# Kernel tuning notes

Hardware: AMD Instinct MI355X
Metric: run time of the kernel (lower is better)

## Reference

```python
import jax, jax.numpy as jnp
import numpy as np

V_F_LEN = 512
I_F_LEN = 256
F_LEN = V_F_LEN + I_F_LEN  # 768, GRU input_size == hidden_size == f_len
NUM_LAYERS = 2
B, S = 64, 256


def _uniform(key, shape, scale):
    return jax.random.uniform(key, shape, jnp.float32, -scale, scale)


def setup_inputs() -> dict:
    key = jax.random.key(0)
    ks = jax.random.split(key, 16)
    fv = jax.random.normal(ks[0], (B, S, V_F_LEN), jnp.float32)
    fi = jax.random.normal(ks[1], (B, S, I_F_LEN), jnp.float32)
    ts = jax.random.uniform(ks[2], (B, S), jnp.float32)
    H = F_LEN
    sc = 1.0 / np.sqrt(H)
    # GRU params, PyTorch layout: [num_layers, 3H, H] with gate order (r, z, n)
    W_ih = _uniform(ks[3], (NUM_LAYERS, 3 * H, H), sc)
    W_hh = _uniform(ks[4], (NUM_LAYERS, 3 * H, H), sc)
    b_ih = _uniform(ks[5], (NUM_LAYERS, 3 * H), sc)
    b_hh = _uniform(ks[6], (NUM_LAYERS, 3 * H), sc)
    sc1 = 1.0 / np.sqrt(H)
    sc2 = 1.0 / np.sqrt(128)
    W1 = _uniform(ks[7], (128, H), sc1)
    b1 = _uniform(ks[8], (128,), sc1)
    W2 = _uniform(ks[9], (6, 128), sc2)
    b2 = _uniform(ks[10], (6,), sc2)
    return {"fv": fv, "fi": fi, "ts": ts, "W_ih": W_ih, "W_hh": W_hh,
            "b_ih": b_ih, "b_hh": b_hh, "W1": W1, "b1": b1, "W2": W2, "b2": b2}


def _gru_layer(x, h0, Wih, Whh, bih, bhh):
    # x: [B, S, H], h0: [B, H]
    def step(h, x_t):
        gi = x_t @ Wih.T + bih          # [B, 3H]
        gh = h @ Whh.T + bhh
        ir, iz, in_ = jnp.split(gi, 3, axis=-1)
        hr, hz, hn = jnp.split(gh, 3, axis=-1)
        r = jax.nn.sigmoid(ir + hr)
        z = jax.nn.sigmoid(iz + hz)
        n = jnp.tanh(in_ + r * hn)
        h_new = (1.0 - z) * n + z * h
        return h_new, h_new
    h_last, ys = jax.lax.scan(step, h0, jnp.swapaxes(x, 0, 1))  # ys: [S, B, H]
    return jnp.swapaxes(ys, 0, 1), h_last


def reference(fv, fi, ts, W_ih, W_hh, b_ih, b_hh, W1, b1, W2, b2):
    # FusionModule with fuse_method='cat': concatenate along feature dim
    fused = jnp.concatenate([fv, fi], axis=-1)  # [B, S, F_LEN]
    bsz = fused.shape[0]
    h0 = jnp.zeros((NUM_LAYERS, bsz, F_LEN), fused.dtype)
    # Note: the torch module feeds one timestep at a time, but the math is
    # identical to running the full sequence through the multilayer GRU.
    x = fused
    h_finals = []
    for l in range(NUM_LAYERS):
        x, h_l = _gru_layer(x, h0[l], W_ih[l], W_hh[l], b_ih[l], b_hh[l])
        h_finals.append(h_l)
    h_n = jnp.stack(h_finals, axis=0)  # [L, B, H]
    hdn = x @ W1.T + b1
    hdn = jnp.where(hdn >= 0, hdn, 0.1 * hdn)  # LeakyReLU(0.1)
    pose = hdn @ W2.T + b2                      # [B, S, 6]
    return (pose, h_n)
```

## Files before the change

kernel.cpp:

```cpp
#include <hip/hip_runtime.h>
#include <stdint.h>


typedef __attribute__((ext_vector_type(8))) short bf16x8;
typedef __attribute__((ext_vector_type(4))) short bf16x4;
typedef __attribute__((ext_vector_type(4))) float f32x4;

#define H_   768
#define TH3  2304
#define BATCH 64
#define SEQ  256
#define SLAB (BATCH * H_)
#define WROW 772
#define FL_STRIDE 128

__device__ __forceinline__ uint16_t f2b(float f) {
  union { float f; uint32_t u; } v; v.f = f;
  uint32_t u = v.u;
  return (uint16_t)((u + 0x7FFFu + ((u >> 16) & 1u)) >> 16);
}

__device__ __forceinline__ f32x4 mfma16(bf16x8 a, bf16x8 b, f32x4 c) {
  return __builtin_amdgcn_mfma_f32_16x16x32_bf16(a, b, c, 0, 0, 0);
}

__device__ __forceinline__ bf16x8 ldB(const uint16_t* p) {
  bf16x4 lo = *reinterpret_cast<const bf16x4*>(p);
  bf16x4 hi = *reinterpret_cast<const bf16x4*>(p + 4);
  bf16x8 r;
  r[0] = lo[0]; r[1] = lo[1]; r[2] = lo[2]; r[3] = lo[3];
  r[4] = hi[0]; r[5] = hi[1]; r[6] = hi[2]; r[7] = hi[3];
  return r;
}

__device__ __forceinline__ void pollFlags48(const int* base, int lane) {
  const int* fp = base + (lane < 48 ? lane : 0);
  int spins = 0;
  for (;;) {
    int v = __hip_atomic_load(fp, __ATOMIC_RELAXED, __HIP_MEMORY_SCOPE_AGENT);
    if (lane >= 48) v = 1;
    if (__all(v != 0)) break;
    if (++spins > (1 << 16)) break;
    __builtin_amdgcn_s_sleep(1);
  }
  __builtin_amdgcn_sched_barrier(0);
}

__device__ __forceinline__ float fsig(float x) {
  return 1.0f / (1.0f + __expf(-x));
}
__device__ __forceinline__ float ftanh(float x) {
  x = fminf(fmaxf(x, -15.0f), 15.0f);
  float e = __expf(2.0f * x);
  return (e - 1.0f) / (e + 1.0f);
}

__global__ __launch_bounds__(256) void prep_kernel(
    const float* __restrict__ fv, const float* __restrict__ fi,
    const float* __restrict__ W1,
    uint16_t* __restrict__ Xbf, int* __restrict__ flags, uint16_t* __restrict__ W1b)
{
  const int NX = SEQ * SLAB;
  const int NC = 257 * FL_STRIDE;
  const int NW = 128 * H_;
  const int total = NX + NC + NW;
  for (int idx = blockIdx.x * blockDim.x + threadIdx.x; idx < total;
       idx += gridDim.x * blockDim.x) {
    if (idx < NX) {
      int s = idx / SLAB;
      int rem = idx - s * SLAB;
      int b = rem / H_;
      int h = rem - b * H_;
      float val = (h < 512) ? fv[((size_t)b * SEQ + s) * 512 + h]
                            : fi[((size_t)b * SEQ + s) * 256 + (h - 512)];
      Xbf[idx] = f2b(val);
    } else if (idx < NX + NC) {
      flags[idx - NX] = 0;
    } else {
      int k = idx - NX - NC;
      W1b[k] = f2b(W1[k]);
    }
  }
}

__global__ __launch_bounds__(512) void gru_persist(
    const float* __restrict__ Wih, const float* __restrict__ Whh,
    const float* __restrict__ bih, const float* __restrict__ bhh,
    const uint16_t* __restrict__ Xbf, uint16_t* __restrict__ Y0, uint16_t* __restrict__ Y1,
    int* __restrict__ flags, float* __restrict__ out_hn)
{
  __shared__ __attribute__((aligned(16))) uint16_t Wx[48 * WROW];
  __shared__ __attribute__((aligned(16))) uint16_t Wh[48 * WROW];
  __shared__ float ghbuf[64 * 48];
  __shared__ float bI[48];
  __shared__ float bH[48];

  const int bid   = blockIdx.x;
  const int slice = bid % 48;
  const int layer = bid / 48;
  const int tid  = threadIdx.x;
  const int lane = tid & 63;
  const int wid  = tid >> 6;
  const int isGh = wid >> 2;
  const int mblk = wid & 3;
  const int n16  = lane & 15;
  const int kg   = lane >> 4;

  const float* wx_g = Wih + (size_t)layer * TH3 * H_;
  const float* wh_g = Whh + (size_t)layer * TH3 * H_;
  for (int idx = tid; idx < 48 * H_; idx += 512) {
    int lr = idx / H_;
    int c  = idx - lr * H_;
    int gate = lr >> 4, j = lr & 15;
    size_t grow = (size_t)(gate * H_ + slice * 16 + j);
    Wx[lr * WROW + c] = f2b(wx_g[grow * H_ + c]);
    Wh[lr * WROW + c] = f2b(wh_g[grow * H_ + c]);
  }
  if (tid < 48) {
    int gate = tid >> 4, j = tid & 15;
    bI[tid] = bih[layer * TH3 + gate * H_ + slice * 16 + j];
    bH[tid] = bhh[layer * TH3 + gate * H_ + slice * 16 + j];
  }
  __syncthreads();

  uint16_t* Yown = layer ? Y1 : Y0;
  const uint16_t* Wh_base = Wh + (size_t)n16 * WROW + kg * 8;
  const uint16_t* Wx_base = Wx + (size_t)n16 * WROW + kg * 8;

  f32x4 xac0 = {0,0,0,0}, xac1 = {0,0,0,0}, xac2 = {0,0,0,0};
  float hp[4] = {0.0f, 0.0f, 0.0f, 0.0f};

  for (int i = 0; i <= 256; ++i) {
    const bool active = (layer == 0) ? (i < 256) : (i >= 1);
    const bool firstA = (layer == 0) ? (i == 0) : (i == 1);

    if (active) {
      if (isGh) {
        if (firstA) {
          #pragma unroll
          for (int q = 0; q < 4; ++q) {
            int bi = mblk * 16 + 4 * kg + q;
            ghbuf[bi * 48 +      n16] = 0.0f;
            ghbuf[bi * 48 + 16 + n16] = 0.0f;
            ghbuf[bi * 48 + 32 + n16] = 0.0f;
          }
        } else {
          pollFlags48(flags + (size_t)(i - 1) * FL_STRIDE + layer * 64, lane);
          const uint16_t* hs = (layer == 0) ? (Y0 + (size_t)i * SLAB)
                                            : (Y1 + (size_t)(i - 1) * SLAB);
          const uint16_t* ap = hs + (size_t)(mblk * 16 + n16) * H_ + kg * 8;
          f32x4 a0 = {0,0,0,0}, a1 = {0,0,0,0}, a2 = {0,0,0,0};
          #pragma unroll
          for (int ks = 0; ks < 24; ++ks) {
            bf16x8 av  = *reinterpret_cast<const bf16x8*>(ap + ks * 32);
            bf16x8 bv0 = ldB(Wh_base + ks * 32);
            bf16x8 bv1 = ldB(Wh_base + 16 * WROW + ks * 32);
            bf16x8 bv2 = ldB(Wh_base + 32 * WROW + ks * 32);
            a0 = mfma16(av, bv0, a0);
            a1 = mfma16(av, bv1, a1);
            a2 = mfma16(av, bv2, a2);
          }
          #pragma unroll
          for (int q = 0; q < 4; ++q) {
            int bi = mblk * 16 + 4 * kg + q;
            ghbuf[bi * 48 +      n16] = a0[q];
            ghbuf[bi * 48 + 16 + n16] = a1[q];
            ghbuf[bi * 48 + 32 + n16] = a2[q];
          }
        }
      } else {
        if (layer == 1) pollFlags48(flags + (size_t)(i - 1) * FL_STRIDE, lane);
        const uint16_t* xs = (layer == 0) ? (Xbf + (size_t)i * SLAB)
                                          : (Y0 + (size_t)i * SLAB);
        const uint16_t* ap = xs + (size_t)(mblk * 16 + n16) * H_ + kg * 8;
        f32x4 a0 = {0,0,0,0}, a1 = {0,0,0,0}, a2 = {0,0,0,0};
        #pragma unroll
        for (int ks = 0; ks < 24; ++ks) {
          bf16x8 av  = *reinterpret_cast<const bf16x8*>(ap + ks * 32);
          bf16x8 bv0 = ldB(Wx_base + ks * 32);
          bf16x8 bv1 = ldB(Wx_base + 16 * WROW + ks * 32);
          bf16x8 bv2 = ldB(Wx_base + 32 * WROW + ks * 32);
          a0 = mfma16(av, bv0, a0);
          a1 = mfma16(av, bv1, a1);
          a2 = mfma16(av, bv2, a2);
        }
        xac0 = a0; xac1 = a1; xac2 = a2;
      }
    }
    __syncthreads();

    if (active && !isGh) {
      uint16_t* dst = Yown + (size_t)((layer == 0) ? (i + 1) : i) * SLAB;
      const bool lastStep = (layer == 0) ? (i == 255) : (i == 256);
      #pragma unroll
      for (int q = 0; q < 4; ++q) {
        int bi = mblk * 16 + 4 * kg + q;
        float ghr = ghbuf[bi * 48 +      n16] + bH[n16];
        float ghz = ghbuf[bi * 48 + 16 + n16] + bH[16 + n16];
        float ghn = ghbuf[bi * 48 + 32 + n16] + bH[32 + n16];
        float gxr = xac0[q] + bI[n16];
        float gxz = xac1[q] + bI[16 + n16];
        float gxn = xac2[q] + bI[32 + n16];
        float rg = fsig(gxr + ghr);
        float zg = fsig(gxz + ghz);
        float ng = ftanh(gxn + rg * ghn);
        float hn2 = (1.0f - zg) * ng + zg * hp[q];
        hp[q] = hn2;
        uint32_t lo = (uint32_t)f2b(hn2);
        uint32_t partner = (uint32_t)__shfl_xor((int)lo, 1, 64);
        if ((n16 & 1) == 0) {
          uint32_t pack = lo | (partner << 16);
          uint32_t* p = (uint32_t*)(dst + (size_t)bi * H_ + slice * 16 + n16);
          __hip_atomic_store(p, pack, __ATOMIC_RELAXED, __HIP_MEMORY_SCOPE_AGENT);
        }
        if (lastStep)
          out_hn[(size_t)layer * SLAB + (size_t)bi * H_ + slice * 16 + n16] = hn2;
      }
      __builtin_amdgcn_s_waitcnt(0);
      __builtin_amdgcn_sched_barrier(0);
    }

    __syncthreads();

    if (i < 256 && tid == 0)
      __hip_atomic_store(&flags[(size_t)i * FL_STRIDE + layer * 64 + slice], 1,
                         __ATOMIC_RELAXED, __HIP_MEMORY_SCOPE_AGENT);
  }
}

__global__ __launch_bounds__(256) void regressor_kernel(
    const uint16_t* __restrict__ Y1, const uint16_t* __restrict__ W1b,
    const float* __restrict__ b1, const float* __restrict__ W2,
    const float* __restrict__ b2, float* __restrict__ pose)
{
  __shared__ float hdn[64 * 132];
  const int t = blockIdx.x;
  const int tid = threadIdx.x;
  const int lane = tid & 63;
  const int wid = tid >> 6;
  const int n16 = lane & 15;
  const int kg = lane >> 4;

  const uint16_t* A  = Y1 + (size_t)(t + 1) * SLAB + (size_t)(wid * 16) * H_;
  const uint16_t* ap = A + (size_t)n16 * H_ + kg * 8;
  const uint16_t* bp = W1b + (size_t)n16 * H_ + kg * 8;

  f32x4 acc[8];
  #pragma unroll
  for (int i = 0; i < 8; ++i) acc[i] = (f32x4){0,0,0,0};

  #pragma unroll
  for (int ks = 0; ks < 24; ++ks) {
    bf16x8 av = *reinterpret_cast<const bf16x8*>(ap + ks * 32);
    #pragma unroll
    for (int nt = 0; nt < 8; ++nt) {
      bf16x8 bv = *reinterpret_cast<const bf16x8*>(bp + (size_t)nt * 16 * H_ + ks * 32);
      acc[nt] = mfma16(av, bv, acc[nt]);
    }
  }
  #pragma unroll
  for (int nt = 0; nt < 8; ++nt) {
    #pragma unroll
    for (int q = 0; q < 4; ++q) {
      int brow = wid * 16 + 4 * kg + q;
      int col  = nt * 16 + n16;
      float v = acc[nt][q] + b1[col];
      v = (v >= 0.0f) ? v : 0.1f * v;
      hdn[brow * 132 + col] = v;
    }
  }
  __syncthreads();
  for (int idx = tid; idx < 384; idx += 256) {
    int b = idx / 6, o = idx % 6;
    const float* w2r = W2 + o * 128;
    const float* hr  = &hdn[b * 132];
    float s = b2[o];
    #pragma unroll 4
    for (int c = 0; c < 128; ++c) s += hr[c] * w2r[c];
    pose[(size_t)b * (SEQ * 6) + (size_t)t * 6 + o] = s;
  }
}

extern "C" void kernel_launch(void* const* d_in, const int* in_sizes, int n_in,
                              void* d_out, int out_size, void* d_ws, size_t ws_size,
                              hipStream_t stream) {
  const float* fv  = (const float*)d_in[0];
  const float* fi  = (const float*)d_in[1];
  const float* Wih = (const float*)d_in[3];
  const float* Whh = (const float*)d_in[4];
  const float* bih = (const float*)d_in[5];
  const float* bhh = (const float*)d_in[6];
  const float* W1  = (const float*)d_in[7];
  const float* b1  = (const float*)d_in[8];
  const float* W2  = (const float*)d_in[9];
  const float* b2  = (const float*)d_in[10];
  float* out = (float*)d_out;

  char* ws = (char*)d_ws;
  size_t off = 0;
  int* flags = (int*)(ws + off);
  off += (size_t)257 * FL_STRIDE * sizeof(int);
  off = (off + 255) & ~(size_t)255;
  uint16_t* Xbf = (uint16_t*)(ws + off); off += (size_t)SEQ * SLAB * 2;
  uint16_t* Y0  = (uint16_t*)(ws + off); off += (size_t)257 * SLAB * 2;
  uint16_t* Y1  = (uint16_t*)(ws + off); off += (size_t)257 * SLAB * 2;
  uint16_t* W1b = (uint16_t*)(ws + off); off += (size_t)128 * H_ * 2;

  prep_kernel<<<2048, 256, 0, stream>>>(fv, fi, W1, Xbf, flags, W1b);
  gru_persist<<<96, 512, 0, stream>>>(Wih, Whh, bih, bhh, Xbf, Y0, Y1, flags, out + 98304);
  regressor_kernel<<<SEQ, 256, 0, stream>>>(Y1, W1b, b1, W2, b2, out);
}
```

Baseline: 2.348 ms.

## Replace per-step block barrier and flag write with LDS counters and vectorized stores

One wave per role now polls the global step flags and hands readiness to the other waves through an LDS variable, so each wave no longer polls global memory on its own. The second __syncthreads per step is dropped: the last gate wave to finish, counted by an LDS atomic, publishes the global flag. New hidden values are staged in LDS and written as 64-bit packed bf16 stores rather than shuffled 32-bit stores. This shortens the serial per-step critical path of the recurrence. The trade-off is extra reliance on the memory ordering of relaxed LDS and global atomics, since ghbuf is reused without a full barrier between steps.

```diff
diff --git a/kernel.cpp b/kernel.cpp
--- a/kernel.cpp
+++ b/kernel.cpp
@@ -42,6 +42,14 @@
     if (__all(v != 0)) break;
     if (++spins > (1 << 16)) break;
     __builtin_amdgcn_s_sleep(1);
+  }
+  __builtin_amdgcn_sched_barrier(0);
+}
+
+__device__ __forceinline__ void ldsSpin(int* addr, int want) {
+  int spins = 0;
+  while (__hip_atomic_load(addr, __ATOMIC_RELAXED, __HIP_MEMORY_SCOPE_WORKGROUP) != want) {
+    if (++spins > (1 << 20)) break;
   }
   __builtin_amdgcn_sched_barrier(0);
 }
@@ -91,9 +99,10 @@
 {
   __shared__ __attribute__((aligned(16))) uint16_t Wx[48 * WROW];
   __shared__ __attribute__((aligned(16))) uint16_t Wh[48 * WROW];
-  __shared__ float ghbuf[64 * 48];
+  __shared__ __attribute__((aligned(16))) float ghbuf[64 * 48];
   __shared__ float bI[48];
   __shared__ float bH[48];
+  __shared__ int ready_h, ready_x, wcnt;
 
   const int bid   = blockIdx.x;
   const int slice = bid % 48;
@@ -106,6 +115,8 @@
   const int n16  = lane & 15;
   const int kg   = lane >> 4;
 
+  if (tid == 0) { ready_h = -1; ready_x = -1; wcnt = 0; }
+
   const float* wx_g = Wih + (size_t)layer * TH3 * H_;
   const float* wh_g = Whh + (size_t)layer * TH3 * H_;
   for (int idx = tid; idx < 48 * H_; idx += 512) {
@@ -145,7 +156,13 @@
             ghbuf[bi * 48 + 32 + n16] = 0.0f;
           }
         } else {
-          pollFlags48(flags + (size_t)(i - 1) * FL_STRIDE + layer * 64, lane);
+          if (wid == 4) {
+            pollFlags48(flags + (size_t)(i - 1) * FL_STRIDE + layer * 64, lane);
+            if (lane == 0)
+              __hip_atomic_store(&ready_h, i, __ATOMIC_RELAXED, __HIP_MEMORY_SCOPE_WORKGROUP);
+          } else {
+            ldsSpin(&ready_h, i);
+          }
           const uint16_t* hs = (layer == 0) ? (Y0 + (size_t)i * SLAB)
                                             : (Y1 + (size_t)(i - 1) * SLAB);
           const uint16_t* ap = hs + (size_t)(mblk * 16 + n16) * H_ + kg * 8;
@@ -169,7 +186,15 @@
           }
         }
       } else {
-        if (layer == 1) pollFlags48(flags + (size_t)(i - 1) * FL_STRIDE, lane);
+        if (layer == 1) {
+          if (wid == 0) {
+            pollFlags48(flags + (size_t)(i - 1) * FL_STRIDE, lane);
+            if (lane == 0)
+              __hip_atomic_store(&ready_x, i, __ATOMIC_RELAXED, __HIP_MEMORY_SCOPE_WORKGROUP);
+          } else {
+            ldsSpin(&ready_x, i);
+          }
+        }
         const uint16_t* xs = (layer == 0) ? (Xbf + (size_t)i * SLAB)
                                           : (Y0 + (size_t)i * SLAB);
         const uint16_t* ap = xs + (size_t)(mblk * 16 + n16) * H_ + kg * 8;
@@ -206,25 +231,37 @@
         float ng = ftanh(gxn + rg * ghn);
         float hn2 = (1.0f - zg) * ng + zg * hp[q];
         hp[q] = hn2;
-        uint32_t lo = (uint32_t)f2b(hn2);
-        uint32_t partner = (uint32_t)__shfl_xor((int)lo, 1, 64);
-        if ((n16 & 1) == 0) {
-          uint32_t pack = lo | (partner << 16);
-          uint32_t* p = (uint32_t*)(dst + (size_t)bi * H_ + slice * 16 + n16);
-          __hip_atomic_store(p, pack, __ATOMIC_RELAXED, __HIP_MEMORY_SCOPE_AGENT);
-        }
+        ghbuf[bi * 48 + n16] = hn2;
+      }
+      __builtin_amdgcn_sched_barrier(0);
+
+      {
+        int row16 = lane & 15;
+        int cg    = lane >> 4;
+        int row   = mblk * 16 + row16;
+        f32x4 v = *reinterpret_cast<const f32x4*>(&ghbuf[row * 48 + cg * 4]);
+        uint64_t u = (uint64_t)f2b(v[0])
+                   | ((uint64_t)f2b(v[1]) << 16)
+                   | ((uint64_t)f2b(v[2]) << 32)
+                   | ((uint64_t)f2b(v[3]) << 48);
+        unsigned long long* p =
+            (unsigned long long*)(dst + (size_t)row * H_ + slice * 16 + cg * 4);
+        __hip_atomic_store(p, u, __ATOMIC_RELAXED, __HIP_MEMORY_SCOPE_AGENT);
         if (lastStep)
-          out_hn[(size_t)layer * SLAB + (size_t)bi * H_ + slice * 16 + n16] = hn2;
+          *reinterpret_cast<f32x4*>(
+              &out_hn[(size_t)layer * SLAB + (size_t)row * H_ + slice * 16 + cg * 4]) = v;
       }
       __builtin_amdgcn_s_waitcnt(0);
       __builtin_amdgcn_sched_barrier(0);
-    }
-
-    __syncthreads();
-
-    if (i < 256 && tid == 0)
-      __hip_atomic_store(&flags[(size_t)i * FL_STRIDE + layer * 64 + slice], 1,
-                         __ATOMIC_RELAXED, __HIP_MEMORY_SCOPE_AGENT);
+      if (lane == 0) {
+        int ret = __hip_atomic_fetch_add(&wcnt, 1, __ATOMIC_RELAXED,
+                                         __HIP_MEMORY_SCOPE_WORKGROUP);
+        int nprev = (layer == 0) ? i : (i - 1);
+        if (ret == nprev * 4 + 3)
+          __hip_atomic_store(&flags[(size_t)i * FL_STRIDE + layer * 64 + slice], 1,
+                             __ATOMIC_RELAXED, __HIP_MEMORY_SCOPE_AGENT);
+      }
+    }
   }
 }
 
```

After: 2.493 ms (median of 2 runs). 6.1% more time.
